# Kernel tuning notes

Hardware: AMD Instinct MI355X
Metric: run time of the kernel (lower is better)

## Reference

```python
import jax, jax.numpy as jnp
import numpy as np

B, S, D = 1, 2048, 2048
H = 16
Q_LORA = 1536
KV_LORA = 512
NOPE = 128
ROPE = 64
VD = 128
QHD = NOPE + ROPE  # 192
THETA = 50000.0
EPS = 1e-6


def rmsnorm(x, w, eps=EPS):
    xf = x.astype(jnp.float32)
    var = jnp.mean(xf * xf, axis=-1, keepdims=True)
    return (w * (xf * jax.lax.rsqrt(var + eps)).astype(x.dtype))


def rotate_half(x):
    x1, x2 = jnp.split(x, 2, axis=-1)
    return jnp.concatenate([-x2, x1], axis=-1)


def deinterleave(x):
    # view(..., d//2, 2).transpose(-1,-2).reshape(..., d): [x0,x2,...,x1,x3,...]
    b, h, s, d = x.shape
    return x.reshape(b, h, s, d // 2, 2).swapaxes(-1, -2).reshape(b, h, s, d)


def setup_inputs() -> dict:
    key = jax.random.key(0)
    ks = jax.random.split(key, 8)
    sc = 0.02
    return {
        "hidden_states": jax.random.normal(ks[0], (B, S, D), jnp.float32),
        "position_ids": jnp.broadcast_to(jnp.arange(S, dtype=jnp.int32), (B, S)),
        "q_a_w": jax.random.normal(ks[1], (Q_LORA, D), jnp.float32) * sc,
        "q_a_ln_w": jnp.ones((Q_LORA,), jnp.float32),
        "q_b_w": jax.random.normal(ks[2], (H * QHD, Q_LORA), jnp.float32) * sc,
        "kv_a_w": jax.random.normal(ks[3], (KV_LORA + ROPE, D), jnp.float32) * sc,
        "kv_a_ln_w": jnp.ones((KV_LORA,), jnp.float32),
        "kv_b_w": jax.random.normal(ks[4], (H * (NOPE + VD), KV_LORA), jnp.float32) * sc,
        "o_w": jax.random.normal(ks[5], (D, H * VD), jnp.float32) * sc,
    }


def reference(hidden_states, position_ids, q_a_w, q_a_ln_w, q_b_w, kv_a_w, kv_a_ln_w, kv_b_w, o_w):
    bsz, q_len, _ = hidden_states.shape
    # low-rank Q: q_b(rmsnorm(q_a(x)))
    q = rmsnorm(hidden_states @ q_a_w.T, q_a_ln_w) @ q_b_w.T
    q = q.reshape(bsz, q_len, H, QHD).transpose(0, 2, 1, 3)  # [b,h,s,192]
    q_nope, q_pe = q[..., :NOPE], q[..., NOPE:]
    # compressed KV + shared rope key
    ckv = hidden_states @ kv_a_w.T  # [b,s,512+64]
    compressed_kv, k_pe = ckv[..., :KV_LORA], ckv[..., KV_LORA:]
    k_pe = k_pe.reshape(bsz, q_len, 1, ROPE).transpose(0, 2, 1, 3)  # [b,1,s,64]
    kv = rmsnorm(compressed_kv, kv_a_ln_w) @ kv_b_w.T
    kv = kv.reshape(bsz, q_len, H, NOPE + VD).transpose(0, 2, 1, 3)
    k_nope, value_states = kv[..., :NOPE], kv[..., NOPE:]
    # rotary cache
    inv_freq = 1.0 / (THETA ** (jnp.arange(0, ROPE, 2, dtype=jnp.float32) / ROPE))
    t = jnp.arange(q_len, dtype=jnp.float32)
    freqs = jnp.outer(t, inv_freq)
    emb = jnp.concatenate([freqs, freqs], axis=-1)  # [s,64]
    cos = jnp.cos(emb)[position_ids][:, None]  # [b,1,s,64]
    sin = jnp.sin(emb)[position_ids][:, None]
    q_pe = deinterleave(q_pe)
    k_pe = deinterleave(k_pe)
    q_pe = q_pe * cos + rotate_half(q_pe) * sin
    k_pe = k_pe * cos + rotate_half(k_pe) * sin
    query_states = jnp.concatenate([q_nope, q_pe], axis=-1)  # [b,h,s,192]
    key_states = jnp.concatenate([k_nope, jnp.broadcast_to(k_pe, (bsz, H, q_len, ROPE))], axis=-1)
    scale = QHD ** (-0.5)
    scores = jnp.einsum('bhqd,bhkd->bhqk', query_states, key_states) * scale
    causal = jnp.tril(jnp.ones((q_len, q_len), bool))
    scores = jnp.where(causal, scores, jnp.finfo(scores.dtype).min)
    attn = jax.nn.softmax(scores, axis=-1)
    out = jnp.einsum('bhqk,bhkd->bhqd', attn, value_states)  # [b,h,s,128]
    out = out.transpose(0, 2, 1, 3).reshape(bsz, q_len, H * VD)
    return out @ o_w.T
```

## Files before the change

kernel.cpp:

```cpp
#include <hip/hip_runtime.h>
#include <hip/hip_bf16.h>
#include <cmath>

#define S_LEN 2048
#define D_MODEL 2048
#define N_HEADS 16
#define Q_LORA 1536
#define KV_LORA 512
#define NOPE 128
#define ROPE_D 64
#define VD 128
#define QHD 192
#define AC_W 2112

typedef __attribute__((ext_vector_type(8))) short bf16x8;
typedef __attribute__((ext_vector_type(4))) float f32x4;
typedef __attribute__((ext_vector_type(4))) unsigned short u16x4;

static __device__ __forceinline__ unsigned short f2u(float x) {
  union { float f; unsigned u; } v; v.f = x;
  unsigned r = v.u + 0x7fffu + ((v.u >> 16) & 1u);
  return (unsigned short)(r >> 16);
}
static __device__ __forceinline__ unsigned short f2u_fast(float x) {
  union { float f; unsigned u; } v; v.f = x;
  return (unsigned short)((v.u + 0x8000u) >> 16);
}
static __device__ __forceinline__ float u2f(unsigned short x) {
  union { unsigned u; float f; } v; v.u = ((unsigned)x) << 16;
  return v.f;
}

#define AS1 __attribute__((address_space(1)))
#define AS3 __attribute__((address_space(3)))
static __device__ __forceinline__ void gload_lds16(const unsigned short* g, unsigned short* l) {
  __builtin_amdgcn_global_load_lds((const AS1 unsigned int*)g, (AS3 unsigned int*)l, 16, 0, 0);
}

__global__ __launch_bounds__(256) void conv_bf16(const float* __restrict__ src,
                                                 unsigned short* __restrict__ dst,
                                                 int n4, float scale) {
  for (int i = blockIdx.x * 256 + threadIdx.x; i < n4; i += gridDim.x * 256) {
    const float4 v = ((const float4*)src)[i];
    u16x4 o;
    o[0] = f2u(v.x * scale); o[1] = f2u(v.y * scale);
    o[2] = f2u(v.z * scale); o[3] = f2u(v.w * scale);
    ((u16x4*)dst)[i] = o;
  }
}

__global__ __launch_bounds__(256) void conv2_bf16(const float* __restrict__ srcA, int n4a,
                                                  const float* __restrict__ srcB, int n4total,
                                                  unsigned short* __restrict__ dst) {
  for (int i = blockIdx.x * 256 + threadIdx.x; i < n4total; i += gridDim.x * 256) {
    const float4 v = (i < n4a) ? ((const float4*)srcA)[i] : ((const float4*)srcB)[i - n4a];
    u16x4 o;
    o[0] = f2u(v.x); o[1] = f2u(v.y); o[2] = f2u(v.z); o[3] = f2u(v.w);
    ((u16x4*)dst)[i] = o;
  }
}

template <int MODE>
__global__ __launch_bounds__(256) void gemm_mfma(const unsigned short* __restrict__ A,
                                                 const unsigned short* __restrict__ W,
                                                 void* __restrict__ Cv,
                                                 unsigned short* __restrict__ C2,
                                                 int N, int K) {
  __shared__ unsigned short As[2][8192];
  __shared__ unsigned short Ws[2][4096];
  const int tid = threadIdx.x;
  const int wave = tid >> 6, lane = tid & 63;
  const int col16 = lane & 15, g = lane >> 4;
  const int arow = blockIdx.y * 128, wrow = blockIdx.x * 64;
  const int wm = (wave >> 1) * 64, wn = (wave & 1) * 32;

  const unsigned short* gA[4];
  const unsigned short* gW[2];
  int dA[4], dW[2];
#pragma unroll
  for (int i = 0; i < 4; ++i) {
    const int c = i * 256 + tid;
    const int r = c >> 3, sl = c & 7;
    gA[i] = A + (size_t)(arow + r) * K + (sl ^ (r & 7)) * 8;
    dA[i] = c * 8;
  }
#pragma unroll
  for (int i = 0; i < 2; ++i) {
    const int c = i * 256 + tid;
    const int r = c >> 3, sl = c & 7;
    gW[i] = W + (size_t)(wrow + r) * K + (sl ^ (r & 7)) * 8;
    dW[i] = c * 8;
  }

  f32x4 acc[4][2];
#pragma unroll
  for (int i = 0; i < 4; ++i)
#pragma unroll
    for (int j = 0; j < 2; ++j) acc[i][j] = (f32x4){0.f, 0.f, 0.f, 0.f};

#pragma unroll
  for (int i = 0; i < 4; ++i) gload_lds16(gA[i], &As[0][dA[i]]);
#pragma unroll
  for (int i = 0; i < 2; ++i) gload_lds16(gW[i], &Ws[0][dW[i]]);

  int cur = 0;
  for (int k0 = 0; k0 < K; k0 += 64) {
    __syncthreads();
    if (k0 + 64 < K) {
      const int b = cur ^ 1, kk = k0 + 64;
#pragma unroll
      for (int i = 0; i < 4; ++i) gload_lds16(gA[i] + kk, &As[b][dA[i]]);
#pragma unroll
      for (int i = 0; i < 2; ++i) gload_lds16(gW[i] + kk, &Ws[b][dW[i]]);
    }
#pragma unroll
    for (int kh = 0; kh < 2; ++kh) {
      bf16x8 af[4], bfr[2];
#pragma unroll
      for (int i = 0; i < 4; ++i) {
        const int row = wm + i * 16 + col16;
        af[i] = *(const bf16x8*)(&As[cur][row * 64 + (((kh * 4 + g) ^ (row & 7)) * 8)]);
      }
#pragma unroll
      for (int j = 0; j < 2; ++j) {
        const int row = wn + j * 16 + col16;
        bfr[j] = *(const bf16x8*)(&Ws[cur][row * 64 + (((kh * 4 + g) ^ (row & 7)) * 8)]);
      }
#pragma unroll
      for (int i = 0; i < 4; ++i)
#pragma unroll
        for (int j = 0; j < 2; ++j)
          acc[i][j] = __builtin_amdgcn_mfma_f32_16x16x32_bf16(af[i], bfr[j], acc[i][j], 0, 0, 0);
    }
    cur ^= 1;
  }

#pragma unroll
  for (int i = 0; i < 4; ++i)
#pragma unroll
    for (int j = 0; j < 2; ++j) {
      const int col = wrow + wn + j * 16 + col16;
      const int row0 = arow + wm + i * 16 + g * 4;
#pragma unroll
      for (int r = 0; r < 4; ++r) {
        if constexpr (MODE == 0)
          ((float*)Cv)[(size_t)(row0 + r) * N + col] = acc[i][j][r];
        else if constexpr (MODE == 1)
          ((unsigned short*)Cv)[(size_t)(row0 + r) * N + col] = f2u(acc[i][j][r]);
        else {
          const int hh = col >> 8, d = col & 255;
          if (d < NOPE)
            C2[((size_t)hh * S_LEN + row0 + r) * QHD + d] = f2u(acc[i][j][r]);
          else
            ((unsigned short*)Cv)[(size_t)(row0 + r) * (N_HEADS * 256) + col] = f2u(acc[i][j][r]);
        }
      }
    }
}

__global__ __launch_bounds__(256) void rmsnorm_kernel(const float* __restrict__ src, int src_ld,
                                                      const float* __restrict__ w,
                                                      unsigned short* __restrict__ dst, int dst_ld,
                                                      int dim) {
  const int row = blockIdx.x;
  const float* x = src + (size_t)row * src_ld;
  float ss = 0.f;
  for (int i = threadIdx.x; i < dim; i += 256) {
    float v = x[i];
    ss += v * v;
  }
#pragma unroll
  for (int off = 32; off; off >>= 1) ss += __shfl_xor(ss, off);
  __shared__ float red[4];
  const int wv = threadIdx.x >> 6, ln = threadIdx.x & 63;
  if (ln == 0) red[wv] = ss;
  __syncthreads();
  const float tot = red[0] + red[1] + red[2] + red[3];
  const float scale = rsqrtf(tot / (float)dim + 1e-6f);
  for (int i = threadIdx.x; i < dim; i += 256) {
    dst[(size_t)row * dst_ld + i] = f2u(w[i] * (x[i] * scale));
  }
}

__global__ void rope_kernel(unsigned short* __restrict__ q, const float* __restrict__ ac,
                            unsigned short* __restrict__ Kb, const int* __restrict__ pos_ids) {
  const int s = blockIdx.x;
  const int j = threadIdx.x;
  const float t = (float)pos_ids[s];
  const float invf = powf(50000.0f, -(float)(2 * j) / 64.0f);
  const float ang = t * invf;
  const float c = cosf(ang), sn = sinf(ang);
  for (int h = 0; h < N_HEADS; ++h) {
    unsigned short* base = q + (size_t)s * (N_HEADS * QHD) + h * QHD + NOPE;
    const float x0 = u2f(base[2 * j]), x1 = u2f(base[2 * j + 1]);
    __syncthreads();
    base[j] = f2u(x0 * c - x1 * sn);
    base[32 + j] = f2u(x1 * c + x0 * sn);
    __syncthreads();
  }
  const float* kb = ac + (size_t)s * AC_W + 2048;
  const unsigned short r0 = f2u(kb[2 * j] * c - kb[2 * j + 1] * sn);
  const unsigned short r1 = f2u(kb[2 * j + 1] * c + kb[2 * j] * sn);
#pragma unroll
  for (int h = 0; h < N_HEADS; ++h) {
    unsigned short* kd = Kb + ((size_t)h * S_LEN + s) * QHD + NOPE;
    kd[j] = r0;
    kd[32 + j] = r1;
  }
}

__global__ __launch_bounds__(256) void build_vt(const unsigned short* __restrict__ kv,
                                                unsigned short* __restrict__ Vt) {
  __shared__ unsigned short t[32][33];
  const int s0 = blockIdx.x * 32, d0 = blockIdx.y * 32, h = blockIdx.z;
  const int tx = threadIdx.x & 31, ty = threadIdx.x >> 5;
#pragma unroll
  for (int i = 0; i < 4; ++i) {
    const int s = s0 + ty + i * 8;
    t[ty + i * 8][tx] = kv[(size_t)s * (N_HEADS * 256) + h * 256 + NOPE + d0 + tx];
  }
  __syncthreads();
  const int p = ((tx & 15) >> 2) * 8 + ((tx >> 4) & 1) * 4 + (tx & 3);
#pragma unroll
  for (int i = 0; i < 4; ++i) {
    const int d = d0 + ty + i * 8;
    Vt[((size_t)h * VD + d) * S_LEN + s0 + p] = t[tx][ty + i * 8];
  }
}

__global__ __launch_bounds__(256, 4) void flash_attn(const unsigned short* __restrict__ Q,
                                                     const unsigned short* __restrict__ Kb,
                                                     const unsigned short* __restrict__ Vt,
                                                     float* __restrict__ O0,
                                                     float* __restrict__ O1,
                                                     float2* __restrict__ ml0,
                                                     float2* __restrict__ ml1) {
  __shared__ unsigned short Ks[2][32 * QHD];
  __shared__ unsigned short Vs[2][VD * 32];
  const int tid = threadIdx.x;
  const int wave = tid >> 6, lane = tid & 63;
  const int g = lane >> 4, col = lane & 15;
  const int lin = (int)blockIdx.x;
  const int h = ((lin & 7) << 1) | ((lin >> 3) & 1);
  const int s = (lin >> 4) & 1;
  const int z = lin >> 5;
  int t;
  if (z < 8) t = 31 - z;
  else if (z < 16) t = z - 8;
  else if (z < 24) t = 39 - z;
  else t = z - 16;
  const int qw = t * 64 + wave * 16;
  const int qr = qw + col;

  bf16x8 qf[6];
  {
    const unsigned short* qrow = Q + (size_t)qr * (N_HEADS * QHD) + h * QHD + g * 8;
#pragma unroll
    for (int i = 0; i < 6; ++i) qf[i] = *(const bf16x8*)(qrow + i * 32);
  }

  const unsigned short* KbH = Kb + (size_t)h * S_LEN * QHD;
  const unsigned short* VtH = Vt + (size_t)h * VD * S_LEN;

  int eK[3], eV[2];
#pragma unroll
  for (int i = 0; i < 3; ++i) {
    const int c = i * 256 + tid;
    const int r = c / 24, sl = c - r * 24;
    eK[i] = r * QHD + (((sl & 24) | ((sl & 7) ^ (r & 7)))) * 8;
  }
#pragma unroll
  for (int i = 0; i < 2; ++i) {
    const int c = i * 256 + tid;
    const int d = c >> 2, sl = c & 3;
    eV[i] = d * S_LEN + ((sl ^ (d & 3))) * 8;
  }

  f32x4 o[8];
#pragma unroll
  for (int i = 0; i < 8; ++i) o[i] = (f32x4){0.f, 0.f, 0.f, 0.f};
  float m = -1e30f, l = 0.f;

  const int nT = t + 1;

  {
    const unsigned short* kp = KbH + (size_t)s * 32 * QHD;
    const unsigned short* vp = VtH + s * 32;
#pragma unroll
    for (int i = 0; i < 3; ++i) gload_lds16(kp + eK[i], &Ks[0][(i * 256 + tid) * 8]);
#pragma unroll
    for (int i = 0; i < 2; ++i) gload_lds16(vp + eV[i], &Vs[0][(i * 256 + tid) * 8]);
  }

  int xK[6];
#pragma unroll
  for (int i = 0; i < 6; ++i) xK[i] = ((4 * i + g) ^ (col & 7)) * 8;
  const int rbK = col * QHD;
  const int xV = (g ^ (col & 3)) * 8;
  const int rbV = col * 32;

  for (int it = 0; it < nT; ++it) {
    __syncthreads();
    if (it + 1 < nT) {
      const int jn = 2 * (it + 1) + s;
      const unsigned short* kp = KbH + (size_t)jn * 32 * QHD;
      const unsigned short* vp = VtH + jn * 32;
      const int b = (it + 1) & 1;
#pragma unroll
      for (int i = 0; i < 3; ++i) gload_lds16(kp + eK[i], &Ks[b][(i * 256 + tid) * 8]);
#pragma unroll
      for (int i = 0; i < 2; ++i) gload_lds16(vp + eV[i], &Vs[b][(i * 256 + tid) * 8]);
    }
    const int k0 = 32 * (2 * it + s);
    if (k0 <= qw + 15) {
      const unsigned short* Ksc = Ks[it & 1];
      const unsigned short* Vsc = Vs[it & 1];

      f32x4 c0 = (f32x4){0.f, 0.f, 0.f, 0.f}, c1 = (f32x4){0.f, 0.f, 0.f, 0.f};
      __builtin_amdgcn_s_setprio(1);
#pragma unroll
      for (int dt = 0; dt < 6; ++dt) {
        const bf16x8 a0 = *(const bf16x8*)(Ksc + rbK + xK[dt]);
        const bf16x8 a1 = *(const bf16x8*)(Ksc + rbK + 16 * QHD + xK[dt]);
        c0 = __builtin_amdgcn_mfma_f32_16x16x32_bf16(a0, qf[dt], c0, 0, 0, 0);
        c1 = __builtin_amdgcn_mfma_f32_16x16x32_bf16(a1, qf[dt], c1, 0, 0, 0);
      }
      __builtin_amdgcn_s_setprio(0);

      if (k0 + 31 > qw) {
#pragma unroll
        for (int r = 0; r < 4; ++r) {
          const int kk = k0 + 4 * g + r;
          if (kk > qr) c0[r] = -1e30f;
          if (kk + 16 > qr) c1[r] = -1e30f;
        }
      }
      float bm = fmaxf(fmaxf(fmaxf(c0[0], c0[1]), fmaxf(c0[2], c0[3])),
                       fmaxf(fmaxf(c1[0], c1[1]), fmaxf(c1[2], c1[3])));
      bm = fmaxf(bm, __shfl_xor(bm, 16));
      bm = fmaxf(bm, __shfl_xor(bm, 32));
      const bool skip = __all(bm <= m + 8.f);
      const float mn = skip ? m : fmaxf(m, bm);
      float ps = 0.f;
      bf16x8 pb;
#pragma unroll
      for (int r = 0; r < 4; ++r) {
        const float p0 = exp2f(c0[r] - mn);
        const float p1 = exp2f(c1[r] - mn);
        ps += p0 + p1;
        pb[r] = (short)f2u_fast(p0);
        pb[4 + r] = (short)f2u_fast(p1);
      }
      ps += __shfl_xor(ps, 16);
      ps += __shfl_xor(ps, 32);
      if (skip) {
        l += ps;
      } else {
        const float corr = exp2f(m - mn);
        l = l * corr + ps;
        m = mn;
#pragma unroll
        for (int i = 0; i < 8; ++i) {
          o[i][0] *= corr; o[i][1] *= corr; o[i][2] *= corr; o[i][3] *= corr;
        }
      }
      __builtin_amdgcn_s_setprio(1);
#pragma unroll
      for (int db = 0; db < 8; ++db) {
        const bf16x8 va = *(const bf16x8*)(Vsc + db * 512 + rbV + xV);
        o[db] = __builtin_amdgcn_mfma_f32_16x16x32_bf16(va, pb, o[db], 0, 0, 0);
      }
      __builtin_amdgcn_s_setprio(0);
    }
  }

  float* Op = s ? O1 : O0;
  float2* mlp = s ? ml1 : ml0;
  float* pr = Op + (size_t)qr * (N_HEADS * VD) + h * VD;
#pragma unroll
  for (int db = 0; db < 8; ++db)
#pragma unroll
    for (int r = 0; r < 4; ++r)
      pr[db * 16 + 4 * g + r] = o[db][r];
  if (g == 0) mlp[qr * N_HEADS + h] = make_float2(m, l);
}

__global__ __launch_bounds__(256) void combine_attn(const float* __restrict__ O0,
                                                    const float* __restrict__ O1,
                                                    const float2* __restrict__ ml0,
                                                    const float2* __restrict__ ml1,
                                                    unsigned short* __restrict__ outb) {
  const int n4 = (S_LEN * N_HEADS * VD) / 4;
  for (int i = blockIdx.x * 256 + threadIdx.x; i < n4; i += gridDim.x * 256) {
    const int e0 = i << 2;
    const int row = e0 >> 11;
    const int h = (e0 >> 7) & 15;
    const float2 a = ml0[row * N_HEADS + h];
    const float2 b = ml1[row * N_HEADS + h];
    const float M = fmaxf(a.x, b.x);
    float wA = exp2f(a.x - M), wB = exp2f(b.x - M);
    const float inv = 1.f / (wA * a.y + wB * b.y);
    wA *= inv; wB *= inv;
    const float4 va = ((const float4*)O0)[i];
    const float4 vb = ((const float4*)O1)[i];
    u16x4 o;
    o[0] = f2u(va.x * wA + vb.x * wB);
    o[1] = f2u(va.y * wA + vb.y * wB);
    o[2] = f2u(va.z * wA + vb.z * wB);
    o[3] = f2u(va.w * wA + vb.w * wB);
    ((u16x4*)outb)[i] = o;
  }
}

extern "C" void kernel_launch(void* const* d_in, const int* in_sizes, int n_in,
                              void* d_out, int out_size, void* d_ws, size_t ws_size,
                              hipStream_t stream) {
  const float* hidden    = (const float*)d_in[0];
  const int*   pos       = (const int*)d_in[1];
  const float* q_a_w     = (const float*)d_in[2];
  const float* q_a_ln_w  = (const float*)d_in[3];
  const float* q_b_w     = (const float*)d_in[4];
  const float* kv_a_w    = (const float*)d_in[5];
  const float* kv_a_ln_w = (const float*)d_in[6];
  const float* kv_b_w    = (const float*)d_in[7];
  const float* o_w       = (const float*)d_in[8];
  float* out = (float*)d_out;
  (void)in_sizes; (void)n_in; (void)out_size; (void)ws_size;

  char* base = (char*)d_ws;
  unsigned short* qbuf  = (unsigned short*)(base);
  unsigned short* kvbuf = (unsigned short*)(base + 12582912);
  float*          O1p   = (float*)(base + 12582912);
  float*          ac    = (float*)(base + 29360128);
  float*          O0p   = (float*)(base + 29360128);
  float2*         ml0   = (float2*)(base + 46661632);
  float2*         ml1   = (float2*)(base + 46923776);
  unsigned short* qan   = (unsigned short*)(base + 46661632);
  unsigned short* ckvn  = (unsigned short*)(base + 52953088);
  unsigned short* Hb    = (unsigned short*)(base + 55050240);
  unsigned short* Vt    = (unsigned short*)(base + 55050240);
  unsigned short* wbuf  = (unsigned short*)(base + 63438848);
  unsigned short* attnb = (unsigned short*)(base + 72876032);
  unsigned short* Kb    = (unsigned short*)(base + 81264640);

  const dim3 b256(256);
  const float qscale = 0.07216878364870323f * 1.4426950408889634f;

  conv_bf16<<<2048, b256, 0, stream>>>(hidden, Hb, (S_LEN * D_MODEL) / 4, 1.f);

  conv2_bf16<<<2048, b256, 0, stream>>>(q_a_w, (Q_LORA * D_MODEL) / 4,
                                        kv_a_w, (AC_W * D_MODEL) / 4, wbuf);
  gemm_mfma<0><<<dim3(AC_W / 64, S_LEN / 128), b256, 0, stream>>>(Hb, wbuf, ac, nullptr, AC_W, D_MODEL);

  rmsnorm_kernel<<<S_LEN, b256, 0, stream>>>(ac, AC_W, q_a_ln_w, qan, Q_LORA, Q_LORA);
  rmsnorm_kernel<<<S_LEN, b256, 0, stream>>>(ac + Q_LORA, AC_W, kv_a_ln_w, ckvn, KV_LORA, KV_LORA);

  conv_bf16<<<2048, b256, 0, stream>>>(q_b_w, wbuf, (N_HEADS * QHD * Q_LORA) / 4, qscale);
  gemm_mfma<1><<<dim3(N_HEADS * QHD / 64, S_LEN / 128), b256, 0, stream>>>(qan, wbuf, qbuf, nullptr, N_HEADS * QHD, Q_LORA);

  conv_bf16<<<2048, b256, 0, stream>>>(kv_b_w, wbuf, (N_HEADS * 256 * KV_LORA) / 4, 1.f);
  gemm_mfma<2><<<dim3(N_HEADS * 256 / 64, S_LEN / 128), b256, 0, stream>>>(ckvn, wbuf, kvbuf, Kb, N_HEADS * 256, KV_LORA);

  rope_kernel<<<S_LEN, 32, 0, stream>>>(qbuf, ac, Kb, pos);

  build_vt<<<dim3(S_LEN / 32, VD / 32, N_HEADS), b256, 0, stream>>>(kvbuf, Vt);

  flash_attn<<<dim3(1024), b256, 0, stream>>>(qbuf, Kb, Vt, O0p, O1p, ml0, ml1);
  combine_attn<<<2048, b256, 0, stream>>>(O0p, O1p, ml0, ml1, attnb);

  conv_bf16<<<2048, b256, 0, stream>>>(o_w, wbuf, (D_MODEL * N_HEADS * VD) / 4, 1.f);
  gemm_mfma<0><<<dim3(D_MODEL / 64, S_LEN / 128), b256, 0, stream>>>(attnb, wbuf, out, nullptr, D_MODEL, N_HEADS * VD);
}
```

Baseline: 208.4 us.

## Use 32x32 MFMA tiles and 4-way KV split in flash attention

Rewrites the flash attention inner loop to use 32x32x16 bf16 MFMA instructions, with each wave owning 32 query rows, and adjusts the V-transpose permutation and K/V swizzles to match. The KV sequence is now split four ways across blocks instead of two, with a new tile schedule, and partial outputs are stored as bf16 rather than fp32. A new combine kernel merges the four partials. The aim is to raise MFMA efficiency and cut partial-output traffic, at the cost of more register pressure (launch bounds relaxed) and extra bf16 rounding of partials.

```diff
diff --git a/kernel.cpp b/kernel.cpp
--- a/kernel.cpp
+++ b/kernel.cpp
@@ -15,6 +15,7 @@
 
 typedef __attribute__((ext_vector_type(8))) short bf16x8;
 typedef __attribute__((ext_vector_type(4))) float f32x4;
+typedef __attribute__((ext_vector_type(16))) float f32x16;
 typedef __attribute__((ext_vector_type(4))) unsigned short u16x4;
 
 static __device__ __forceinline__ unsigned short f2u(float x) {
@@ -220,7 +221,10 @@
     t[ty + i * 8][tx] = kv[(size_t)s * (N_HEADS * 256) + h * 256 + NOPE + d0 + tx];
   }
   __syncthreads();
-  const int p = ((tx & 15) >> 2) * 8 + ((tx >> 4) & 1) * 4 + (tx & 3);
+  const int g16 = tx >> 4, k16 = tx & 15;
+  const int h2 = (k16 >> 2) & 1;
+  const int jj = (k16 & 3) + 4 * ((k16 >> 3) & 1);
+  const int p = g16 * 16 + h2 * 8 + jj;
 #pragma unroll
   for (int i = 0; i < 4; ++i) {
     const int d = d0 + ty + i * 8;
@@ -228,35 +232,30 @@
   }
 }
 
-__global__ __launch_bounds__(256, 4) void flash_attn(const unsigned short* __restrict__ Q,
-                                                     const unsigned short* __restrict__ Kb,
-                                                     const unsigned short* __restrict__ Vt,
-                                                     float* __restrict__ O0,
-                                                     float* __restrict__ O1,
-                                                     float2* __restrict__ ml0,
-                                                     float2* __restrict__ ml1) {
+__global__ __launch_bounds__(256) void flash_attn(const unsigned short* __restrict__ Q,
+                                                  const unsigned short* __restrict__ Kb,
+                                                  const unsigned short* __restrict__ Vt,
+                                                  unsigned short* __restrict__ Pb,
+                                                  float2* __restrict__ mlb) {
   __shared__ unsigned short Ks[2][32 * QHD];
   __shared__ unsigned short Vs[2][VD * 32];
   const int tid = threadIdx.x;
   const int wave = tid >> 6, lane = tid & 63;
-  const int g = lane >> 4, col = lane & 15;
+  const int q5 = lane & 31, h2 = lane >> 5;
   const int lin = (int)blockIdx.x;
   const int h = ((lin & 7) << 1) | ((lin >> 3) & 1);
-  const int s = (lin >> 4) & 1;
-  const int z = lin >> 5;
-  int t;
-  if (z < 8) t = 31 - z;
-  else if (z < 16) t = z - 8;
-  else if (z < 24) t = 39 - z;
-  else t = z - 16;
-  const int qw = t * 64 + wave * 16;
-  const int qr = qw + col;
-
-  bf16x8 qf[6];
+  const int s = (lin >> 4) & 3;
+  const int z = lin >> 6;
+  const int za = z >> 2, zb = z & 3;
+  const int t = 4 * za + ((za + zb) & 3);
+  const int qw = t * 128 + wave * 32;
+  const int qr = qw + q5;
+
+  bf16x8 qf[12];
   {
-    const unsigned short* qrow = Q + (size_t)qr * (N_HEADS * QHD) + h * QHD + g * 8;
-#pragma unroll
-    for (int i = 0; i < 6; ++i) qf[i] = *(const bf16x8*)(qrow + i * 32);
+    const unsigned short* qrow = Q + (size_t)qr * (N_HEADS * QHD) + h * QHD + h2 * 8;
+#pragma unroll
+    for (int i = 0; i < 12; ++i) qf[i] = *(const bf16x8*)(qrow + i * 16);
   }
 
   const unsigned short* KbH = Kb + (size_t)h * S_LEN * QHD;
@@ -276,9 +275,21 @@
     eV[i] = d * S_LEN + ((sl ^ (d & 3))) * 8;
   }
 
-  f32x4 o[8];
-#pragma unroll
-  for (int i = 0; i < 8; ++i) o[i] = (f32x4){0.f, 0.f, 0.f, 0.f};
+  int xK[12];
+#pragma unroll
+  for (int i = 0; i < 12; ++i) {
+    const int sg = 2 * i + h2;
+    xK[i] = q5 * QHD + (((sg & 24) | ((sg & 7) ^ (q5 & 7)))) * 8;
+  }
+  int xV[2];
+#pragma unroll
+  for (int i = 0; i < 2; ++i) xV[i] = q5 * 32 + (((i * 2 + h2) ^ (q5 & 3))) * 8;
+
+  f32x16 o[4];
+#pragma unroll
+  for (int i = 0; i < 4; ++i)
+#pragma unroll
+    for (int r = 0; r < 16; ++r) o[i][r] = 0.f;
   float m = -1e30f, l = 0.f;
 
   const int nT = t + 1;
@@ -292,17 +303,10 @@
     for (int i = 0; i < 2; ++i) gload_lds16(vp + eV[i], &Vs[0][(i * 256 + tid) * 8]);
   }
 
-  int xK[6];
-#pragma unroll
-  for (int i = 0; i < 6; ++i) xK[i] = ((4 * i + g) ^ (col & 7)) * 8;
-  const int rbK = col * QHD;
-  const int xV = (g ^ (col & 3)) * 8;
-  const int rbV = col * 32;
-
   for (int it = 0; it < nT; ++it) {
     __syncthreads();
     if (it + 1 < nT) {
-      const int jn = 2 * (it + 1) + s;
+      const int jn = 4 * (it + 1) + s;
       const unsigned short* kp = KbH + (size_t)jn * 32 * QHD;
       const unsigned short* vp = VtH + jn * 32;
       const int b = (it + 1) & 1;
@@ -311,47 +315,45 @@
 #pragma unroll
       for (int i = 0; i < 2; ++i) gload_lds16(vp + eV[i], &Vs[b][(i * 256 + tid) * 8]);
     }
-    const int k0 = 32 * (2 * it + s);
-    if (k0 <= qw + 15) {
+    const int k0 = 32 * (4 * it + s);
+    if (k0 <= qw + 31) {
       const unsigned short* Ksc = Ks[it & 1];
       const unsigned short* Vsc = Vs[it & 1];
 
-      f32x4 c0 = (f32x4){0.f, 0.f, 0.f, 0.f}, c1 = (f32x4){0.f, 0.f, 0.f, 0.f};
+      f32x16 c;
+#pragma unroll
+      for (int r = 0; r < 16; ++r) c[r] = 0.f;
       __builtin_amdgcn_s_setprio(1);
 #pragma unroll
-      for (int dt = 0; dt < 6; ++dt) {
-        const bf16x8 a0 = *(const bf16x8*)(Ksc + rbK + xK[dt]);
-        const bf16x8 a1 = *(const bf16x8*)(Ksc + rbK + 16 * QHD + xK[dt]);
-        c0 = __builtin_amdgcn_mfma_f32_16x16x32_bf16(a0, qf[dt], c0, 0, 0, 0);
-        c1 = __builtin_amdgcn_mfma_f32_16x16x32_bf16(a1, qf[dt], c1, 0, 0, 0);
+      for (int dt = 0; dt < 12; ++dt) {
+        const bf16x8 a = *(const bf16x8*)(Ksc + xK[dt]);
+        c = __builtin_amdgcn_mfma_f32_32x32x16_bf16(a, qf[dt], c, 0, 0, 0);
       }
       __builtin_amdgcn_s_setprio(0);
 
       if (k0 + 31 > qw) {
 #pragma unroll
-        for (int r = 0; r < 4; ++r) {
-          const int kk = k0 + 4 * g + r;
-          if (kk > qr) c0[r] = -1e30f;
-          if (kk + 16 > qr) c1[r] = -1e30f;
+        for (int r = 0; r < 16; ++r) {
+          const int kk = k0 + (r & 3) + 8 * (r >> 2) + 4 * h2;
+          if (kk > qr) c[r] = -1e30f;
         }
       }
-      float bm = fmaxf(fmaxf(fmaxf(c0[0], c0[1]), fmaxf(c0[2], c0[3])),
-                       fmaxf(fmaxf(c1[0], c1[1]), fmaxf(c1[2], c1[3])));
-      bm = fmaxf(bm, __shfl_xor(bm, 16));
+      float bm = c[0];
+#pragma unroll
+      for (int r = 1; r < 16; ++r) bm = fmaxf(bm, c[r]);
       bm = fmaxf(bm, __shfl_xor(bm, 32));
       const bool skip = __all(bm <= m + 8.f);
       const float mn = skip ? m : fmaxf(m, bm);
       float ps = 0.f;
-      bf16x8 pb;
-#pragma unroll
-      for (int r = 0; r < 4; ++r) {
-        const float p0 = exp2f(c0[r] - mn);
-        const float p1 = exp2f(c1[r] - mn);
+      bf16x8 pb0, pb1;
+#pragma unroll
+      for (int r = 0; r < 8; ++r) {
+        const float p0 = exp2f(c[r] - mn);
+        const float p1 = exp2f(c[8 + r] - mn);
         ps += p0 + p1;
-        pb[r] = (short)f2u_fast(p0);
-        pb[4 + r] = (short)f2u_fast(p1);
-      }
-      ps += __shfl_xor(ps, 16);
+        pb0[r] = (short)f2u_fast(p0);
+        pb1[r] = (short)f2u_fast(p1);
+      }
       ps += __shfl_xor(ps, 32);
       if (skip) {
         l += ps;
@@ -360,56 +362,72 @@
         l = l * corr + ps;
         m = mn;
 #pragma unroll
-        for (int i = 0; i < 8; ++i) {
-          o[i][0] *= corr; o[i][1] *= corr; o[i][2] *= corr; o[i][3] *= corr;
-        }
+        for (int i = 0; i < 4; ++i)
+#pragma unroll
+          for (int r = 0; r < 16; ++r) o[i][r] *= corr;
       }
       __builtin_amdgcn_s_setprio(1);
 #pragma unroll
-      for (int db = 0; db < 8; ++db) {
-        const bf16x8 va = *(const bf16x8*)(Vsc + db * 512 + rbV + xV);
-        o[db] = __builtin_amdgcn_mfma_f32_16x16x32_bf16(va, pb, o[db], 0, 0, 0);
+      for (int db = 0; db < 4; ++db) {
+        const bf16x8 va0 = *(const bf16x8*)(Vsc + db * 1024 + xV[0]);
+        o[db] = __builtin_amdgcn_mfma_f32_32x32x16_bf16(va0, pb0, o[db], 0, 0, 0);
+        const bf16x8 va1 = *(const bf16x8*)(Vsc + db * 1024 + xV[1]);
+        o[db] = __builtin_amdgcn_mfma_f32_32x32x16_bf16(va1, pb1, o[db], 0, 0, 0);
       }
       __builtin_amdgcn_s_setprio(0);
     }
   }
 
-  float* Op = s ? O1 : O0;
-  float2* mlp = s ? ml1 : ml0;
-  float* pr = Op + (size_t)qr * (N_HEADS * VD) + h * VD;
-#pragma unroll
-  for (int db = 0; db < 8; ++db)
-#pragma unroll
-    for (int r = 0; r < 4; ++r)
-      pr[db * 16 + 4 * g + r] = o[db][r];
-  if (g == 0) mlp[qr * N_HEADS + h] = make_float2(m, l);
-}
-
-__global__ __launch_bounds__(256) void combine_attn(const float* __restrict__ O0,
-                                                    const float* __restrict__ O1,
-                                                    const float2* __restrict__ ml0,
-                                                    const float2* __restrict__ ml1,
-                                                    unsigned short* __restrict__ outb) {
-  const int n4 = (S_LEN * N_HEADS * VD) / 4;
-  for (int i = blockIdx.x * 256 + threadIdx.x; i < n4; i += gridDim.x * 256) {
-    const int e0 = i << 2;
-    const int row = e0 >> 11;
-    const int h = (e0 >> 7) & 15;
-    const float2 a = ml0[row * N_HEADS + h];
-    const float2 b = ml1[row * N_HEADS + h];
-    const float M = fmaxf(a.x, b.x);
-    float wA = exp2f(a.x - M), wB = exp2f(b.x - M);
-    const float inv = 1.f / (wA * a.y + wB * b.y);
-    wA *= inv; wB *= inv;
-    const float4 va = ((const float4*)O0)[i];
-    const float4 vb = ((const float4*)O1)[i];
-    u16x4 o;
-    o[0] = f2u(va.x * wA + vb.x * wB);
-    o[1] = f2u(va.y * wA + vb.y * wB);
-    o[2] = f2u(va.z * wA + vb.z * wB);
-    o[3] = f2u(va.w * wA + vb.w * wB);
-    ((u16x4*)outb)[i] = o;
-  }
+  unsigned short* pr = Pb + (((size_t)qr * 4 + s) * N_HEADS + h) * VD;
+#pragma unroll
+  for (int db = 0; db < 4; ++db)
+#pragma unroll
+    for (int rq = 0; rq < 4; ++rq) {
+      const int d0 = db * 32 + 4 * h2 + 8 * rq;
+      u16x4 w4;
+      w4[0] = f2u(o[db][rq * 4 + 0]);
+      w4[1] = f2u(o[db][rq * 4 + 1]);
+      w4[2] = f2u(o[db][rq * 4 + 2]);
+      w4[3] = f2u(o[db][rq * 4 + 3]);
+      *(uint2*)(pr + d0) = __builtin_bit_cast(uint2, w4);
+    }
+  if (h2 == 0) mlb[((size_t)qr * 4 + s) * N_HEADS + h] = make_float2(m, l);
+}
+
+__global__ __launch_bounds__(256) void combine4(const unsigned short* __restrict__ Pb,
+                                                const float2* __restrict__ mlb,
+                                                unsigned short* __restrict__ outb) {
+  const int idx = blockIdx.x * 256 + threadIdx.x;
+  const int d8 = idx & 15, hq = idx >> 4;
+  const int h = hq & 15, q = hq >> 4;
+  float2 ml[4];
+  float M = -1e30f;
+#pragma unroll
+  for (int s = 0; s < 4; ++s) {
+    ml[s] = mlb[((size_t)q * 4 + s) * N_HEADS + h];
+    M = fmaxf(M, ml[s].x);
+  }
+  float w[4], den = 0.f;
+#pragma unroll
+  for (int s = 0; s < 4; ++s) {
+    w[s] = exp2f(ml[s].x - M);
+    den += w[s] * ml[s].y;
+  }
+  const float inv = 1.f / den;
+  float acc[8] = {};
+#pragma unroll
+  for (int s = 0; s < 4; ++s) {
+    const bf16x8 v = *(const bf16x8*)(Pb + (((size_t)q * 4 + s) * N_HEADS + h) * VD + d8 * 8);
+    const float ws = w[s] * inv;
+#pragma unroll
+    for (int e = 0; e < 8; ++e) acc[e] += u2f((unsigned short)v[e]) * ws;
+  }
+  u16x4 o0, o1;
+#pragma unroll
+  for (int e = 0; e < 4; ++e) { o0[e] = f2u(acc[e]); o1[e] = f2u(acc[4 + e]); }
+  unsigned short* dst = outb + ((size_t)q * N_HEADS + h) * VD + d8 * 8;
+  *(uint2*)(dst) = __builtin_bit_cast(uint2, o0);
+  *(uint2*)(dst + 4) = __builtin_bit_cast(uint2, o1);
 }
 
 extern "C" void kernel_launch(void* const* d_in, const int* in_sizes, int n_in,
@@ -430,11 +448,9 @@
   char* base = (char*)d_ws;
   unsigned short* qbuf  = (unsigned short*)(base);
   unsigned short* kvbuf = (unsigned short*)(base + 12582912);
-  float*          O1p   = (float*)(base + 12582912);
+  unsigned short* Pbuf  = (unsigned short*)(base + 12582912);
+  float2*         mlb   = (float2*)(base + 46137344);
   float*          ac    = (float*)(base + 29360128);
-  float*          O0p   = (float*)(base + 29360128);
-  float2*         ml0   = (float2*)(base + 46661632);
-  float2*         ml1   = (float2*)(base + 46923776);
   unsigned short* qan   = (unsigned short*)(base + 46661632);
   unsigned short* ckvn  = (unsigned short*)(base + 52953088);
   unsigned short* Hb    = (unsigned short*)(base + 55050240);
@@ -465,8 +481,8 @@
 
   build_vt<<<dim3(S_LEN / 32, VD / 32, N_HEADS), b256, 0, stream>>>(kvbuf, Vt);
 
-  flash_attn<<<dim3(1024), b256, 0, stream>>>(qbuf, Kb, Vt, O0p, O1p, ml0, ml1);
-  combine_attn<<<2048, b256, 0, stream>>>(O0p, O1p, ml0, ml1, attnb);
+  flash_attn<<<dim3(1024), b256, 0, stream>>>(qbuf, Kb, Vt, Pbuf, mlb);
+  combine4<<<2048, b256, 0, stream>>>(Pbuf, mlb, attnb);
 
   conv_bf16<<<2048, b256, 0, stream>>>(o_w, wbuf, (D_MODEL * N_HEADS * VD) / 4, 1.f);
   gemm_mfma<0><<<dim3(D_MODEL / 64, S_LEN / 128), b256, 0, stream>>>(attnb, wbuf, out, nullptr, D_MODEL, N_HEADS * VD);
```

Result: slower. 213.4 us (+2.4%).
